# Performance work log

Hardware: AMD Instinct MI355X
Metric: run time of the kernel (lower is better)

## Reference

```python
import jax, jax.numpy as jnp
import numpy as np

N = 131072          # number of input points
M = 512             # num_prototypes
D = 64              # feature_dim
GAMMA = 1.0


def setup_inputs() -> dict:
    key = jax.random.key(0)
    kx, kp = jax.random.split(key)
    x = jax.random.normal(kx, (N, D), dtype=jnp.float32)
    prototypes = jax.random.normal(kp, (M, D), dtype=jnp.float32)
    return {"x": x, "prototypes": prototypes}


def reference(x, prototypes):
    x_sq = jnp.sum(x * x, axis=-1, keepdims=True)            # [N, 1]
    p_sq = jnp.sum(prototypes * prototypes, axis=-1)         # [M]
    cross = jnp.einsum('nd,md->nm', x, prototypes)           # [N, M]
    dist2 = x_sq + p_sq[None, :] - 2.0 * cross               # [N, M]
    dist2 = jnp.maximum(dist2, 0.0)                          # guard tiny negatives
    return jnp.exp(-GAMMA * dist2)
```

## Files before the change

### kernel.cpp

```cpp
#include <hip/hip_runtime.h>
#include <hip/hip_bf16.h>


#define N_PTS 131072
#define M_PROT 512
#define D_DIM 64
#define BN 128
#define BM 128
#define NCHUNK (M_PROT / BM)

#define FMA4(a, s, v)                \
  {                                  \
    (a).x = fmaf((s), (v).x, (a).x); \
    (a).y = fmaf((s), (v).y, (a).y); \
    (a).z = fmaf((s), (v).z, (a).z); \
    (a).w = fmaf((s), (v).w, (a).w); \
  }

__global__ __launch_bounds__(256, 2)
void rbf_kernel(const float* __restrict__ x,
                const float* __restrict__ prot,
                float* __restrict__ out) {
  __shared__ float xT[D_DIM][BN];
  __shared__ float pT[D_DIM][BM];
  __shared__ float xs[BN];
  __shared__ float ps[BM];

  const int tid = threadIdx.x;
  const int tx = tid & 15;
  const int ty = tid >> 4;
  const int n0 = blockIdx.x * BN;

#pragma unroll
  for (int i = 0; i < 8; ++i) {
    const int idx = tid + i * 256;
    const int r  = idx >> 4;
    const int c4 = idx & 15;
    const float4 v = *reinterpret_cast<const float4*>(x + (size_t)(n0 + r) * D_DIM + c4 * 4);
    xT[c4 * 4 + 0][r] = v.x;
    xT[c4 * 4 + 1][r] = v.y;
    xT[c4 * 4 + 2][r] = v.z;
    xT[c4 * 4 + 3][r] = v.w;
  }

  for (int mc = 0; mc < NCHUNK; ++mc) {
#pragma unroll
    for (int i = 0; i < 8; ++i) {
      const int idx = tid + i * 256;
      const int r  = idx >> 4;
      const int c4 = idx & 15;
      const float4 v =
          *reinterpret_cast<const float4*>(prot + (size_t)(mc * BM + r) * D_DIM + c4 * 4);
      pT[c4 * 4 + 0][r] = v.x;
      pT[c4 * 4 + 1][r] = v.y;
      pT[c4 * 4 + 2][r] = v.z;
      pT[c4 * 4 + 3][r] = v.w;
    }
    __syncthreads();

    if (mc == 0 && tid < BN) {
      float s = 0.f;
#pragma unroll 8
      for (int d = 0; d < D_DIM; ++d) {
        const float v = xT[d][tid];
        s = fmaf(v, v, s);
      }
      xs[tid] = s;
    }
    if (tid >= 128) {
      const int m = tid - 128;
      float s = 0.f;
#pragma unroll 8
      for (int d = 0; d < D_DIM; ++d) {
        const float v = pT[d][m];
        s = fmaf(v, v, s);
      }
      ps[m] = s;
    }

    float4 acc[8][2];
#pragma unroll
    for (int i = 0; i < 8; ++i) {
      acc[i][0] = make_float4(0.f, 0.f, 0.f, 0.f);
      acc[i][1] = make_float4(0.f, 0.f, 0.f, 0.f);
    }

#pragma unroll 4
    for (int d = 0; d < D_DIM; ++d) {
      const float4 xa = *reinterpret_cast<const float4*>(&xT[d][ty * 8]);
      const float4 xb = *reinterpret_cast<const float4*>(&xT[d][ty * 8 + 4]);
      const float4 p0 = *reinterpret_cast<const float4*>(&pT[d][tx * 4]);
      const float4 p1 = *reinterpret_cast<const float4*>(&pT[d][64 + tx * 4]);
      const float xsc[8] = {xa.x, xa.y, xa.z, xa.w, xb.x, xb.y, xb.z, xb.w};
#pragma unroll
      for (int i = 0; i < 8; ++i) {
        FMA4(acc[i][0], xsc[i], p0);
        FMA4(acc[i][1], xsc[i], p1);
      }
    }
    __syncthreads();

    const int mbase = mc * BM;
#pragma unroll
    for (int i = 0; i < 8; ++i) {
      const int n = n0 + ty * 8 + i;
      const float xsn = xs[ty * 8 + i];
#pragma unroll
      for (int g = 0; g < 2; ++g) {
        const float4 psv = *reinterpret_cast<const float4*>(&ps[g * 64 + tx * 4]);
        const float4 a = acc[i][g];
        float4 r;
        r.x = __expf(fminf(fmaf(2.f, a.x, -xsn) - psv.x, 0.f));
        r.y = __expf(fminf(fmaf(2.f, a.y, -xsn) - psv.y, 0.f));
        r.z = __expf(fminf(fmaf(2.f, a.z, -xsn) - psv.z, 0.f));
        r.w = __expf(fminf(fmaf(2.f, a.w, -xsn) - psv.w, 0.f));
        *reinterpret_cast<float4*>(out + (size_t)n * M_PROT + mbase + g * 64 + tx * 4) = r;
      }
    }
  }
}

extern "C" void kernel_launch(void* const* d_in, const int* in_sizes, int n_in,
                              void* d_out, int out_size, void* d_ws, size_t ws_size,
                              hipStream_t stream) {
  const float* x = (const float*)d_in[0];
  const float* p = (const float*)d_in[1];
  float* out = (float*)d_out;
  (void)in_sizes; (void)n_in; (void)out_size; (void)d_ws; (void)ws_size;
  rbf_kernel<<<N_PTS / BN, 256, 0, stream>>>(x, p, out);
}
```

Before: 371.8 us.

## Compute RBF cross term with bf16x3 split MFMA and 2D block grid

Replaces the FP32 scalar-FMA outer-product GEMM with MFMA bf16 16x16x32 instructions, splitting each fp32 operand into high and low bf16 parts and summing three products to keep near-fp32 accuracy. The grid now tiles both N and M, giving four times as many blocks, each handling one 128x128 tile instead of looping over all prototype chunks. Squared norms are computed directly from global memory. Output stores become scalar, strided by rows per lane, rather than float4, which may hurt write coalescing on this write-bound kernel.

```diff
diff --git a/kernel.cpp b/kernel.cpp
--- a/kernel.cpp
+++ b/kernel.cpp
@@ -7,114 +7,132 @@
 #define D_DIM 64
 #define BN 128
 #define BM 128
-#define NCHUNK (M_PROT / BM)
+#define LDP 72
 
-#define FMA4(a, s, v)                \
-  {                                  \
-    (a).x = fmaf((s), (v).x, (a).x); \
-    (a).y = fmaf((s), (v).y, (a).y); \
-    (a).z = fmaf((s), (v).z, (a).z); \
-    (a).w = fmaf((s), (v).w, (a).w); \
-  }
+typedef __attribute__((ext_vector_type(8))) short short8;
+typedef __attribute__((ext_vector_type(4))) float f32x4;
+
+__device__ inline ushort f2bf(float f) {
+  uint u = __float_as_uint(f);
+  uint r = (u + 0x7FFFu + ((u >> 16) & 1u)) >> 16;
+  return (ushort)r;
+}
+__device__ inline float bf2f(ushort h) { return __uint_as_float(((uint)h) << 16); }
+
+__device__ inline void split4(float4 v, uint2& hp, uint2& lp) {
+  ushort h0 = f2bf(v.x), h1 = f2bf(v.y), h2 = f2bf(v.z), h3 = f2bf(v.w);
+  ushort l0 = f2bf(v.x - bf2f(h0));
+  ushort l1 = f2bf(v.y - bf2f(h1));
+  ushort l2 = f2bf(v.z - bf2f(h2));
+  ushort l3 = f2bf(v.w - bf2f(h3));
+  hp.x = (uint)h0 | ((uint)h1 << 16);
+  hp.y = (uint)h2 | ((uint)h3 << 16);
+  lp.x = (uint)l0 | ((uint)l1 << 16);
+  lp.y = (uint)l2 | ((uint)l3 << 16);
+}
 
 __global__ __launch_bounds__(256, 2)
-void rbf_kernel(const float* __restrict__ x,
-                const float* __restrict__ prot,
-                float* __restrict__ out) {
-  __shared__ float xT[D_DIM][BN];
-  __shared__ float pT[D_DIM][BM];
-  __shared__ float xs[BN];
-  __shared__ float ps[BM];
+void rbf_mfma(const float* __restrict__ x,
+              const float* __restrict__ prot,
+              float* __restrict__ out) {
+  __shared__ ushort XH[BN][LDP], XL[BN][LDP];
+  __shared__ ushort PH[BM][LDP], PL[BM][LDP];
+  __shared__ float XS[BN], PS[BM];
 
   const int tid = threadIdx.x;
-  const int tx = tid & 15;
-  const int ty = tid >> 4;
-  const int n0 = blockIdx.x * BN;
+  const int bid = blockIdx.x;
+  const int n0 = (bid >> 2) * BN;
+  const int m0 = (bid & 3) * BM;
 
 #pragma unroll
   for (int i = 0; i < 8; ++i) {
     const int idx = tid + i * 256;
-    const int r  = idx >> 4;
+    const int r = idx >> 4;
     const int c4 = idx & 15;
     const float4 v = *reinterpret_cast<const float4*>(x + (size_t)(n0 + r) * D_DIM + c4 * 4);
-    xT[c4 * 4 + 0][r] = v.x;
-    xT[c4 * 4 + 1][r] = v.y;
-    xT[c4 * 4 + 2][r] = v.z;
-    xT[c4 * 4 + 3][r] = v.w;
+    uint2 hp, lp;
+    split4(v, hp, lp);
+    *reinterpret_cast<uint2*>(&XH[r][c4 * 4]) = hp;
+    *reinterpret_cast<uint2*>(&XL[r][c4 * 4]) = lp;
+  }
+#pragma unroll
+  for (int i = 0; i < 8; ++i) {
+    const int idx = tid + i * 256;
+    const int r = idx >> 4;
+    const int c4 = idx & 15;
+    const float4 v = *reinterpret_cast<const float4*>(prot + (size_t)(m0 + r) * D_DIM + c4 * 4);
+    uint2 hp, lp;
+    split4(v, hp, lp);
+    *reinterpret_cast<uint2*>(&PH[r][c4 * 4]) = hp;
+    *reinterpret_cast<uint2*>(&PL[r][c4 * 4]) = lp;
   }
 
-  for (int mc = 0; mc < NCHUNK; ++mc) {
+  {
+    const int r = tid & 127;
+    const float* src = (tid < 128) ? (x + (size_t)(n0 + r) * D_DIM)
+                                   : (prot + (size_t)(m0 + r) * D_DIM);
+    float s = 0.f;
 #pragma unroll
-    for (int i = 0; i < 8; ++i) {
-      const int idx = tid + i * 256;
-      const int r  = idx >> 4;
-      const int c4 = idx & 15;
-      const float4 v =
-          *reinterpret_cast<const float4*>(prot + (size_t)(mc * BM + r) * D_DIM + c4 * 4);
-      pT[c4 * 4 + 0][r] = v.x;
-      pT[c4 * 4 + 1][r] = v.y;
-      pT[c4 * 4 + 2][r] = v.z;
-      pT[c4 * 4 + 3][r] = v.w;
+    for (int c = 0; c < 16; ++c) {
+      const float4 v = *reinterpret_cast<const float4*>(src + c * 4);
+      s = fmaf(v.x, v.x, s);
+      s = fmaf(v.y, v.y, s);
+      s = fmaf(v.z, v.z, s);
+      s = fmaf(v.w, v.w, s);
     }
-    __syncthreads();
+    if (tid < 128) XS[r] = s; else PS[r] = s;
+  }
+  __syncthreads();
 
-    if (mc == 0 && tid < BN) {
-      float s = 0.f;
-#pragma unroll 8
-      for (int d = 0; d < D_DIM; ++d) {
-        const float v = xT[d][tid];
-        s = fmaf(v, v, s);
+  const int lane = tid & 63;
+  const int wave = tid >> 6;
+  const int wr = wave >> 1, wc = wave & 1;
+  const int lrow = lane & 15;
+  const int kg16 = (lane >> 4) * 8;
+
+  f32x4 acc[4][4];
+#pragma unroll
+  for (int i = 0; i < 4; ++i)
+#pragma unroll
+    for (int j = 0; j < 4; ++j)
+      acc[i][j] = (f32x4){0.f, 0.f, 0.f, 0.f};
+
+#pragma unroll
+  for (int s = 0; s < 3; ++s) {
+    const ushort(*A)[LDP] = (s == 2) ? XL : XH;
+    const ushort(*B)[LDP] = (s == 1) ? PL : PH;
+#pragma unroll
+    for (int h = 0; h < 2; ++h) {
+      const int d0 = h * 32 + kg16;
+      short8 a[4], b[4];
+#pragma unroll
+      for (int f = 0; f < 4; ++f) {
+        a[f] = *reinterpret_cast<const short8*>(&A[wr * 64 + f * 16 + lrow][d0]);
+        b[f] = *reinterpret_cast<const short8*>(&B[wc * 64 + f * 16 + lrow][d0]);
       }
-      xs[tid] = s;
-    }
-    if (tid >= 128) {
-      const int m = tid - 128;
-      float s = 0.f;
-#pragma unroll 8
-      for (int d = 0; d < D_DIM; ++d) {
-        const float v = pT[d][m];
-        s = fmaf(v, v, s);
+#pragma unroll
+      for (int i = 0; i < 4; ++i)
+#pragma unroll
+        for (int j = 0; j < 4; ++j)
+          acc[i][j] = __builtin_amdgcn_mfma_f32_16x16x32_bf16(a[i], b[j], acc[i][j], 0, 0, 0);
       }
-      ps[m] = s;
-    }
+  }
 
-    float4 acc[8][2];
+  const int rloc = wr * 64 + (lane >> 4) * 4;
+  const int cloc = wc * 64 + (lane & 15);
 #pragma unroll
-    for (int i = 0; i < 8; ++i) {
-      acc[i][0] = make_float4(0.f, 0.f, 0.f, 0.f);
-      acc[i][1] = make_float4(0.f, 0.f, 0.f, 0.f);
-    }
-
-#pragma unroll 4
-    for (int d = 0; d < D_DIM; ++d) {
-      const float4 xa = *reinterpret_cast<const float4*>(&xT[d][ty * 8]);
-      const float4 xb = *reinterpret_cast<const float4*>(&xT[d][ty * 8 + 4]);
-      const float4 p0 = *reinterpret_cast<const float4*>(&pT[d][tx * 4]);
-      const float4 p1 = *reinterpret_cast<const float4*>(&pT[d][64 + tx * 4]);
-      const float xsc[8] = {xa.x, xa.y, xa.z, xa.w, xb.x, xb.y, xb.z, xb.w};
+  for (int i = 0; i < 4; ++i) {
 #pragma unroll
-      for (int i = 0; i < 8; ++i) {
-        FMA4(acc[i][0], xsc[i], p0);
-        FMA4(acc[i][1], xsc[i], p1);
-      }
-    }
-    __syncthreads();
-
-    const int mbase = mc * BM;
+    for (int j = 0; j < 4; ++j) {
+      const f32x4 c = acc[i][j];
+      const int col = cloc + j * 16;
+      const float psv = PS[col];
+      float* outp = out + (size_t)(n0 + rloc + i * 16) * M_PROT + (m0 + col);
 #pragma unroll
-    for (int i = 0; i < 8; ++i) {
-      const int n = n0 + ty * 8 + i;
-      const float xsn = xs[ty * 8 + i];
-#pragma unroll
-      for (int g = 0; g < 2; ++g) {
-        const float4 psv = *reinterpret_cast<const float4*>(&ps[g * 64 + tx * 4]);
-        const float4 a = acc[i][g];
-        float4 r;
-        r.x = __expf(fminf(fmaf(2.f, a.x, -xsn) - psv.x, 0.f));
-        r.y = __expf(fminf(fmaf(2.f, a.y, -xsn) - psv.y, 0.f));
-        r.z = __expf(fminf(fmaf(2.f, a.z, -xsn) - psv.z, 0.f));
-        r.w = __expf(fminf(fmaf(2.f, a.w, -xsn) - psv.w, 0.f));
-        *reinterpret_cast<float4*>(out + (size_t)n * M_PROT + mbase + g * 64 + tx * 4) = r;
+      for (int r = 0; r < 4; ++r) {
+        const float xsv = XS[rloc + i * 16 + r];
+        const float e = fminf(fmaf(2.f, c[r], -xsv) - psv, 0.f);
+        outp[(size_t)r * M_PROT] = __expf(e);
       }
     }
   }
@@ -127,5 +145,5 @@
   const float* p = (const float*)d_in[1];
   float* out = (float*)d_out;
   (void)in_sizes; (void)n_in; (void)out_size; (void)d_ws; (void)ws_size;
-  rbf_kernel<<<N_PTS / BN, 256, 0, stream>>>(x, p, out);
+  rbf_mfma<<<dim3((N_PTS / BN) * (M_PROT / BM)), 256, 0, stream>>>(x, p, out);
 }
```

Measured after the change: 342.7 us. -7.8%, faster.
